# Kernel tuning notes

Measured on AMD Instinct MI355X. Metric: run time of the kernel, lower is better.

The kernel has to match this reference:

```python
import jax, jax.numpy as jnp
import numpy as np

N_NODES = 50000
N_EDGES = 500000


def setup_inputs() -> dict:
    key = jax.random.key(0)
    ks = jax.random.split(key, 24)
    p = {}
    p['x_feat'] = jax.random.normal(ks[0], (N_NODES, 24), dtype=jnp.float32)
    p['edge_index'] = jax.random.randint(ks[1], (2, N_EDGES), 0, N_NODES)
    p['edge_attr'] = jax.random.uniform(ks[2], (N_EDGES, 16), dtype=jnp.float32)
    def lin(k, fan_in, shape):
        b = 1.0 / np.sqrt(fan_in)
        return jax.random.uniform(k, shape, jnp.float32, -b, b)
    # group-0 input projection: 24 -> 32
    p['lin_prep_W'] = lin(ks[3], 24, (24, 32)); p['lin_prep_b'] = lin(ks[4], 24, (32,))
    # prep tube: 32 -> 16
    p['tube_W'] = lin(ks[5], 32, (32, 16)); p['tube_b'] = lin(ks[6], 32, (16,))
    # shared edge-attr trunk: 16 -> 32 -> 16
    p['edge_W1'] = lin(ks[7], 16, (16, 32)); p['edge_b1'] = lin(ks[8], 16, (32,))
    p['edge_W2'] = lin(ks[9], 32, (32, 16)); p['edge_b2'] = lin(ks[10], 32, (16,))
    # conv1: in=16, out=8 per aggr (mean, max, add)
    p['conv1_edge_W'] = lin(ks[11], 16, (3, 16, 16 * 8)); p['conv1_edge_b'] = lin(ks[12], 16, (3, 16 * 8))
    p['conv1_root_W'] = lin(ks[13], 16, (3, 16, 8)); p['conv1_bias'] = lin(ks[14], 16, (3, 8))
    # conv2: in=24, out=8 per aggr
    p['conv2_edge_W'] = lin(ks[15], 16, (3, 16, 24 * 8)); p['conv2_edge_b'] = lin(ks[16], 16, (3, 24 * 8))
    p['conv2_root_W'] = lin(ks[17], 24, (3, 24, 8)); p['conv2_bias'] = lin(ks[18], 24, (3, 8))
    # output head: 24 -> 2
    p['out_W'] = lin(ks[19], 24, (24, 2)); p['out_b'] = lin(ks[20], 24, (2,))
    return p


def _nnconv(x, e_repr, src, dst, edge_W, edge_b, root_W, bias, n_nodes):
    # x: [N, in]; e_repr: [E, 16]; edge_W: [3, 16, in*out]
    d_in = x.shape[1]
    x_src = x[src]  # [E, in]
    deg = jax.ops.segment_sum(jnp.ones_like(src, dtype=x.dtype), dst, num_segments=n_nodes)  # [N]
    outs = []
    for a, aggr in enumerate(('mean', 'max', 'add')):
        W_e = (e_repr @ edge_W[a] + edge_b[a]).reshape(e_repr.shape[0], d_in, -1)  # [E, in, out]
        msg = jnp.einsum('ei,eio->eo', x_src, W_e)  # [E, out]
        if aggr == 'add':
            agg = jax.ops.segment_sum(msg, dst, num_segments=n_nodes)
        elif aggr == 'mean':
            agg = jax.ops.segment_sum(msg, dst, num_segments=n_nodes) / jnp.maximum(deg, 1.0)[:, None]
        else:
            agg = jax.ops.segment_max(msg, dst, num_segments=n_nodes)
            agg = jnp.where(deg[:, None] > 0, agg, 0.0)  # no-neighbor nodes -> 0
        outs.append(agg + x @ root_W[a] + bias[a])
    return jax.nn.relu(jnp.concatenate(outs, axis=1))  # [N, 3*out]


def reference(x_feat, edge_index, edge_attr, lin_prep_W, lin_prep_b, tube_W, tube_b,
              edge_W1, edge_b1, edge_W2, edge_b2,
              conv1_edge_W, conv1_edge_b, conv1_root_W, conv1_bias,
              conv2_edge_W, conv2_edge_b, conv2_root_W, conv2_bias,
              out_W, out_b):
    n_nodes = x_feat.shape[0]
    src, dst = edge_index[0], edge_index[1]
    # node prep: group projection + tube (relu acts, dropout=0 -> identity)
    x = jax.nn.relu(x_feat @ lin_prep_W + lin_prep_b)       # [N, 32]
    x = jax.nn.relu(x @ tube_W + tube_b)                    # [N, 16]
    # shared edge-attr trunk (last activation = sigmoid), computed once
    e = jax.nn.relu(edge_attr @ edge_W1 + edge_b1)
    e_repr = jax.nn.sigmoid(e @ edge_W2 + edge_b2)          # [E, 16]
    # hop 1 and hop 2 of edge-conditioned NNConv with mean/max/add aggregators
    x = _nnconv(x, e_repr, src, dst, conv1_edge_W, conv1_edge_b, conv1_root_W, conv1_bias, n_nodes)  # [N, 24]
    x = _nnconv(x, e_repr, src, dst, conv2_edge_W, conv2_edge_b, conv2_root_W, conv2_bias, n_nodes)  # [N, 24]
    logits = x @ out_W + out_b                              # [N, 2]
    scores = jax.nn.softmax(logits, axis=1)
    return (logits, scores)
```

## Files before the change

### kernel.cpp

```cpp
#include <hip/hip_runtime.h>

#define BS 256

__device__ __forceinline__ unsigned short f2bf(float f) {
    unsigned x = __float_as_uint(f);
    return (unsigned short)((x + 0x7fffu + ((x >> 16) & 1u)) >> 16);
}
__device__ __forceinline__ unsigned pack2bf(float a, float b) {
    return (unsigned)f2bf(a) | ((unsigned)f2bf(b) << 16);
}
__device__ __forceinline__ void unpack2(unsigned u, float* d) {
    d[0] = __uint_as_float(u << 16);
    d[1] = __uint_as_float(u & 0xFFFF0000u);
}
__device__ __forceinline__ void unpack8(uint4 v, float* d) {
    unpack2(v.x, d); unpack2(v.y, d + 2); unpack2(v.z, d + 4); unpack2(v.w, d + 6);
}
__device__ __forceinline__ uint4 pack8bf(const float* r) {
    return make_uint4(pack2bf(r[0], r[1]), pack2bf(r[2], r[3]),
                      pack2bf(r[4], r[5]), pack2bf(r[6], r[7]));
}

__global__ void prep_kernel(const float* __restrict__ xf,
                            const float* __restrict__ W1, const float* __restrict__ b1,
                            const float* __restrict__ W2, const float* __restrict__ b2,
                            float* __restrict__ x16, int N)
{
    int n = blockIdx.x * blockDim.x + threadIdx.x;
    bool valid = n < N;
    int nn = valid ? n : 0;
    float a[24];
#pragma unroll
    for (int i = 0; i < 24; i += 4)
        *(float4*)(a + i) = *(const float4*)(xf + (size_t)nn * 24 + i);
    float h[32];
#pragma unroll
    for (int j = 0; j < 32; j++) {
        float s = b1[j];
#pragma unroll
        for (int i = 0; i < 24; i++) s = fmaf(a[i], W1[i * 32 + j], s);
        h[j] = fmaxf(s, 0.f);
    }
    if (!valid) return;
#pragma unroll
    for (int j = 0; j < 16; j++) {
        float s = b2[j];
#pragma unroll
        for (int i = 0; i < 32; i++) s = fmaf(h[i], W2[i * 16 + j], s);
        x16[(size_t)n * 16 + j] = fmaxf(s, 0.f);
    }
}

__global__ void degjj_kernel(const int* __restrict__ srcA, const int* __restrict__ dstA,
                             int* __restrict__ cntS, int* __restrict__ cntD,
                             int* __restrict__ jS, int* __restrict__ jD, int E)
{
    int base = blockIdx.x * (BS * 4) + threadIdx.x;
    int e0 = base, e1 = base + BS, e2 = base + 2 * BS, e3 = base + 3 * BS;
    bool v0 = e0 < E, v1 = e1 < E, v2 = e2 < E, v3 = e3 < E;
    int s0 = 0, s1 = 0, s2 = 0, s3 = 0, d0 = 0, d1 = 0, d2 = 0, d3 = 0;
    if (v0) { s0 = srcA[e0]; d0 = dstA[e0]; }
    if (v1) { s1 = srcA[e1]; d1 = dstA[e1]; }
    if (v2) { s2 = srcA[e2]; d2 = dstA[e2]; }
    if (v3) { s3 = srcA[e3]; d3 = dstA[e3]; }
    int a0 = 0, a1 = 0, a2 = 0, a3 = 0, b0 = 0, b1 = 0, b2 = 0, b3 = 0;
    if (v0) { a0 = atomicAdd(&cntS[s0], 1); b0 = atomicAdd(&cntD[d0], 1); }
    if (v1) { a1 = atomicAdd(&cntS[s1], 1); b1 = atomicAdd(&cntD[d1], 1); }
    if (v2) { a2 = atomicAdd(&cntS[s2], 1); b2 = atomicAdd(&cntD[d2], 1); }
    if (v3) { a3 = atomicAdd(&cntS[s3], 1); b3 = atomicAdd(&cntD[d3], 1); }
    if (v0) { jS[e0] = a0; jD[e0] = b0; }
    if (v1) { jS[e1] = a1; jD[e1] = b1; }
    if (v2) { jS[e2] = a2; jD[e2] = b2; }
    if (v3) { jS[e3] = a3; jD[e3] = b3; }
}

__global__ void offsets2_kernel(const int* __restrict__ cntS, const int* __restrict__ cntD,
                                int* __restrict__ offsS, int* __restrict__ offsD,
                                int* __restrict__ cursS, int* __restrict__ cursD, int N)
{
    int n = blockIdx.x * blockDim.x + threadIdx.x;
    int lane = threadIdx.x & 63;
    bool valid = n < N;
    int dS = valid ? cntS[n] : 0;
    int dD = valid ? cntD[n] : 0;
    int sS = dS, sD = dD;
#pragma unroll
    for (int o = 1; o < 64; o <<= 1) {
        int tS = __shfl_up(sS, o);
        int tD = __shfl_up(sD, o);
        if (lane >= o) { sS += tS; sD += tD; }
    }
    int totS = __shfl(sS, 63);
    int totD = __shfl(sD, 63);
    int baseS = 0, baseD = 0;
    if (lane == 63) {
        baseS = atomicAdd(cursS, totS);
        baseD = atomicAdd(cursD, totD);
    }
    baseS = __shfl(baseS, 63);
    baseD = __shfl(baseD, 63);
    if (valid) {
        offsS[n] = baseS + sS - dS;
        offsD[n] = baseD + sD - dD;
    }
}

__global__ __launch_bounds__(BS) void er_fill_kernel(
    const int* __restrict__ srcA, const int* __restrict__ dstA,
    const int* __restrict__ jS, const int* __restrict__ jD,
    const int* __restrict__ offsS, const int* __restrict__ offsD,
    const float* __restrict__ eattr,
    const float* __restrict__ eW1, const float* __restrict__ eb1,
    const float* __restrict__ eW2, const float* __restrict__ eb2,
    uint4* __restrict__ erec, int E)
{
    int e = blockIdx.x * BS + threadIdx.x;
    if (e >= E) return;
    int s = srcA[e], d = dstA[e];
    int p = offsS[s] + jS[e];
    int q = offsD[d] + jD[e];

    float ea[16];
#pragma unroll
    for (int i = 0; i < 16; i += 4)
        *(float4*)(ea + i) = *(const float4*)(eattr + (size_t)e * 16 + i);
    float h[32];
#pragma unroll
    for (int j = 0; j < 32; j++) {
        float t = eb1[j];
#pragma unroll
        for (int i = 0; i < 16; i++) t = fmaf(ea[i], eW1[i * 32 + j], t);
        h[j] = fmaxf(t, 0.f);
    }
    float er[16];
#pragma unroll
    for (int j = 0; j < 16; j++) {
        float t = eb2[j];
#pragma unroll
        for (int i = 0; i < 32; i++) t = fmaf(h[i], eW2[i * 16 + j], t);
        er[j] = 1.f / (1.f + __expf(-t));
    }
    unsigned w[8];
#pragma unroll
    for (int j = 0; j < 8; j++) w[j] = pack2bf(er[2 * j], er[2 * j + 1]);
    uint4* rp = erec + (size_t)p * 4;
    rp[0] = make_uint4((unsigned)s, (unsigned)q, w[0], w[1]);
    rp[1] = make_uint4(w[2], w[3], w[4], w[5]);
    rp[2] = make_uint4(w[6], w[7], 0u, 0u);
    rp[3] = make_uint4(0u, 0u, 0u, 0u);
}

template <int IN>
__global__ __launch_bounds__(BS) void ynode_kernel(const float* __restrict__ x,
                                                   const float* __restrict__ W,
                                                   const float* __restrict__ B,
                                                   const float* __restrict__ RW,
                                                   const float* __restrict__ RB,
                                                   unsigned short* __restrict__ Y,
                                                   float* __restrict__ root, int N)
{
    __shared__ float w_lds[IN * 24];
    int t = threadIdx.x;
    int k = blockIdx.y;

    for (int idx = t; idx < IN * 24; idx += BS) {
        int i = idx / 24;
        int j = idx - i * 24;
        int a = j >> 3, o = j & 7;
        float v;
        if (k < 16)       v = W[(((size_t)a * 16 + k) * IN + i) * 8 + o];
        else if (k == 16) v = B[((size_t)a * IN + i) * 8 + o];
        else              v = RW[((size_t)a * IN + i) * 8 + o];
        w_lds[idx] = v;
    }
    __syncthreads();

    int tid = blockIdx.x * BS + t;
    int n = tid / 3;
    int a = tid - n * 3;
    if (n >= N) return;

    float xv[IN];
#pragma unroll
    for (int i = 0; i < IN; i += 4)
        *(float4*)(xv + i) = *(const float4*)(x + (size_t)n * IN + i);

    float acc[8];
#pragma unroll
    for (int o = 0; o < 8; o++) acc[o] = 0.f;
    const float* wb = w_lds + a * 8;
#pragma unroll
    for (int i = 0; i < IN; i++) {
        float xi = xv[i];
#pragma unroll
        for (int o = 0; o < 8; o++)
            acc[o] = fmaf(xi, wb[i * 24 + o], acc[o]);
    }

    if (k < 17) {
        *(uint4*)(Y + ((size_t)k * N + n) * 24 + a * 8) = pack8bf(acc);
    } else {
        float* pr = root + (size_t)n * 24 + a * 8;
        *(float4*)(pr)     = make_float4(acc[0] + RB[a*8+0], acc[1] + RB[a*8+1],
                                         acc[2] + RB[a*8+2], acc[3] + RB[a*8+3]);
        *(float4*)(pr + 4) = make_float4(acc[4] + RB[a*8+4], acc[5] + RB[a*8+5],
                                         acc[6] + RB[a*8+6], acc[7] + RB[a*8+7]);
    }
}

__global__ __launch_bounds__(BS) void msg_kernel(
    const uint4* __restrict__ erec,
    const unsigned short* __restrict__ Y,
    unsigned short* __restrict__ msg16,
    int N, int E)
{
    int tid = blockIdx.x * BS + threadIdx.x;
    int p = tid / 3;
    int j = tid - p * 3;
    if (p >= E) return;

    const uint4* rp = erec + (size_t)p * 4;
    uint4 r0 = rp[0];
    uint4 r1 = rp[1];
    uint4 r2 = rp[2];
    unsigned s = r0.x, q = r0.y;

    float er[16];
    unpack2(r0.z, er); unpack2(r0.w, er + 2);
    unpack8(r1, er + 4);
    unpack2(r2.x, er + 12); unpack2(r2.y, er + 14);

    const unsigned short* yb = Y + (size_t)s * 24 + j * 8;
    size_t kstride = (size_t)N * 24;

    float acc[8];
    unpack8(*(const uint4*)(yb + 16 * kstride), acc);
#pragma unroll
    for (int k = 0; k < 16; k++) {
        float t[8];
        unpack8(*(const uint4*)(yb + (size_t)k * kstride), t);
        float ek = er[k];
#pragma unroll
        for (int o = 0; o < 8; o++) acc[o] = fmaf(ek, t[o], acc[o]);
    }
    unsigned short* mrow = msg16 + (size_t)q * 32;
    *(uint4*)(mrow + j * 8) = pack8bf(acc);
    if (j == 0) *(uint4*)(mrow + 24) = make_uint4(0, 0, 0, 0);
}

__global__ __launch_bounds__(BS) void gather_kernel(
    const unsigned short* __restrict__ msg16,
    const int* __restrict__ offs,
    const int* __restrict__ degi,
    const float* __restrict__ root,
    float* __restrict__ out, int N)
{
    int n = (blockIdx.x * BS + threadIdx.x) >> 6;
    if (n >= N) return;
    int lane = threadIdx.x & 63;
    int c = lane & 3;
    int r = lane >> 2;

    int off = offs[n];
    int d = degi[n];

    float s[8], m[8];
#pragma unroll
    for (int o = 0; o < 8; o++) { s[o] = 0.f; m[o] = -3.402823466e38f; }

    if (c < 3) {
        const unsigned short* base = msg16 + (size_t)off * 32 + c * 8;
        for (int j = r; j < d; j += 16) {
            uint4 v = *(const uint4*)(base + (size_t)j * 32);
            float t[8];
            unpack8(v, t);
#pragma unroll
            for (int o = 0; o < 8; o++) {
                s[o] += t[o];
                m[o] = fmaxf(m[o], t[o]);
            }
        }
    }
#pragma unroll
    for (int mask = 4; mask < 64; mask <<= 1) {
#pragma unroll
        for (int o = 0; o < 8; o++) {
            s[o] += __shfl_xor(s[o], mask);
            m[o] = fmaxf(m[o], __shfl_xor(m[o], mask));
        }
    }
    if (lane >= 3) return;

    float inv = 1.f / fmaxf((float)d, 1.f);
    const float* pr = root + (size_t)n * 24 + c * 8;
    float4 r0 = *(const float4*)(pr);
    float4 r1 = *(const float4*)(pr + 4);
    float rb[8] = {r0.x, r0.y, r0.z, r0.w, r1.x, r1.y, r1.z, r1.w};
    float rr[8];
#pragma unroll
    for (int o = 0; o < 8; o++) {
        float agg = (c == 0) ? s[o] * inv
                  : (c == 1) ? ((d > 0) ? m[o] : 0.f)
                  : s[o];
        rr[o] = fmaxf(rb[o] + agg, 0.f);
    }
    float* po = out + (size_t)n * 24 + c * 8;
    *(float4*)(po)     = make_float4(rr[0], rr[1], rr[2], rr[3]);
    *(float4*)(po + 4) = make_float4(rr[4], rr[5], rr[6], rr[7]);
}

__global__ void head_kernel(const float* __restrict__ x, const float* __restrict__ W,
                            const float* __restrict__ b, float* __restrict__ out, int N)
{
    int n = blockIdx.x * blockDim.x + threadIdx.x;
    if (n >= N) return;
    float l0 = b[0], l1 = b[1];
#pragma unroll
    for (int i = 0; i < 24; i++) {
        float xi = x[(size_t)n * 24 + i];
        l0 = fmaf(xi, W[i * 2 + 0], l0);
        l1 = fmaf(xi, W[i * 2 + 1], l1);
    }
    out[2 * (size_t)n + 0] = l0;
    out[2 * (size_t)n + 1] = l1;
    float mx = fmaxf(l0, l1);
    float e0 = __expf(l0 - mx), e1 = __expf(l1 - mx);
    float sm = e0 + e1;
    out[2 * (size_t)N + 2 * (size_t)n + 0] = e0 / sm;
    out[2 * (size_t)N + 2 * (size_t)n + 1] = e1 / sm;
}

extern "C" void kernel_launch(void* const* d_in, const int* in_sizes, int n_in,
                              void* d_out, int out_size, void* d_ws, size_t ws_size,
                              hipStream_t stream)
{
    const float* x_feat = (const float*)d_in[0];
    const int*   eidx   = (const int*)d_in[1];
    const float* eattr  = (const float*)d_in[2];
    const float* lpW = (const float*)d_in[3];
    const float* lpb = (const float*)d_in[4];
    const float* tW  = (const float*)d_in[5];
    const float* tb  = (const float*)d_in[6];
    const float* eW1 = (const float*)d_in[7];
    const float* eb1 = (const float*)d_in[8];
    const float* eW2 = (const float*)d_in[9];
    const float* eb2 = (const float*)d_in[10];
    const float* c1W = (const float*)d_in[11];
    const float* c1B = (const float*)d_in[12];
    const float* c1R = (const float*)d_in[13];
    const float* c1b = (const float*)d_in[14];
    const float* c2W = (const float*)d_in[15];
    const float* c2B = (const float*)d_in[16];
    const float* c2R = (const float*)d_in[17];
    const float* c2b = (const float*)d_in[18];
    const float* oW  = (const float*)d_in[19];
    const float* ob  = (const float*)d_in[20];

    int N = in_sizes[0] / 24;
    int E = in_sizes[1] / 2;
    const int* srcA = eidx;
    const int* dstA = eidx + E;

    char* wsb = (char*)d_ws;
    size_t off = 0;
    auto alloc = [&](size_t bytes) {
        off = (off + 255) & ~(size_t)255;
        void* p = wsb + off;
        off += bytes;
        return p;
    };
    unsigned short* Y     = (unsigned short*)alloc((size_t)17 * N * 24 * 2);
    unsigned short* msg16 = (unsigned short*)alloc((size_t)E * 32 * 2);
    uint4* erec = (uint4*)alloc((size_t)E * 64);
    float* root = (float*)alloc((size_t)N * 24 * 4);
    float* x16  = (float*)alloc((size_t)N * 16 * 4);
    float* x24a = (float*)alloc((size_t)N * 24 * 4);
    float* x24b = (float*)alloc((size_t)N * 24 * 4);
    int* ibase  = (int*)alloc(((size_t)2 * N + 2) * 4);
    int* cntS = ibase;
    int* cntD = ibase + N;
    int* cursS = ibase + 2 * N;
    int* cursD = ibase + 2 * N + 1;
    int* offsS = (int*)alloc((size_t)N * 4);
    int* offsD = (int*)alloc((size_t)N * 4);
    int* jS    = (int*)alloc((size_t)E * 4);
    int* jD    = (int*)alloc((size_t)E * 4);

    dim3 blk(BS);
    int nb_nodes = (N + BS - 1) / BS;
    int nb_edges = (E + BS - 1) / BS;
    int nb_deg   = (E + BS * 4 - 1) / (BS * 4);
    int nb_msg   = (3 * E + BS - 1) / BS;
    int nb_gath  = ((size_t)N * 64 + BS - 1) / BS;
    int nb_y3    = (3 * N + BS - 1) / BS;
    dim3 ygrid(nb_y3, 18);

    hipMemsetAsync(ibase, 0, (2 * (size_t)N + 2) * 4, stream);

    prep_kernel<<<nb_nodes, blk, 0, stream>>>(x_feat, lpW, lpb, tW, tb, x16, N);

    degjj_kernel<<<nb_deg, blk, 0, stream>>>(srcA, dstA, cntS, cntD, jS, jD, E);
    offsets2_kernel<<<nb_nodes, blk, 0, stream>>>(cntS, cntD, offsS, offsD, cursS, cursD, N);
    er_fill_kernel<<<nb_edges, blk, 0, stream>>>(srcA, dstA, jS, jD, offsS, offsD,
                                                 eattr, eW1, eb1, eW2, eb2, erec, E);

    ynode_kernel<16><<<ygrid, blk, 0, stream>>>(x16, c1W, c1B, c1R, c1b, Y, root, N);
    msg_kernel<<<nb_msg, blk, 0, stream>>>(erec, Y, msg16, N, E);
    gather_kernel<<<nb_gath, blk, 0, stream>>>(msg16, offsD, cntD, root, x24a, N);

    ynode_kernel<24><<<ygrid, blk, 0, stream>>>(x24a, c2W, c2B, c2R, c2b, Y, root, N);
    msg_kernel<<<nb_msg, blk, 0, stream>>>(erec, Y, msg16, N, E);
    gather_kernel<<<nb_gath, blk, 0, stream>>>(msg16, offsD, cntD, root, x24b, N);

    head_kernel<<<nb_nodes, blk, 0, stream>>>(x24b, oW, ob, (float*)d_out, N);
}
```

Measured before the change: 284.9 us.

## Fuse prep with degree counting, head into final gather, and batch edge MLP

Merges the node prep MLP and the degree/rank atomic counting into one launch, split by block index. The degree counting now uses one atomic per thread over 2E threads instead of four edges per thread. The output head and softmax are folded into the second gather kernel through cross-lane shuffles, which removes one launch and the x24b round trip. The edge MLP kernel now handles two edges per thread so each weight load is reused, at the cost of more registers per thread.

```diff
diff --git a/kernel.cpp b/kernel.cpp
--- a/kernel.cpp
+++ b/kernel.cpp
@@ -21,57 +21,49 @@
                       pack2bf(r[4], r[5]), pack2bf(r[6], r[7]));
 }
 
-__global__ void prep_kernel(const float* __restrict__ xf,
-                            const float* __restrict__ W1, const float* __restrict__ b1,
-                            const float* __restrict__ W2, const float* __restrict__ b2,
-                            float* __restrict__ x16, int N)
-{
-    int n = blockIdx.x * blockDim.x + threadIdx.x;
-    bool valid = n < N;
-    int nn = valid ? n : 0;
-    float a[24];
-#pragma unroll
-    for (int i = 0; i < 24; i += 4)
-        *(float4*)(a + i) = *(const float4*)(xf + (size_t)nn * 24 + i);
-    float h[32];
-#pragma unroll
-    for (int j = 0; j < 32; j++) {
-        float s = b1[j];
-#pragma unroll
-        for (int i = 0; i < 24; i++) s = fmaf(a[i], W1[i * 32 + j], s);
-        h[j] = fmaxf(s, 0.f);
-    }
-    if (!valid) return;
-#pragma unroll
-    for (int j = 0; j < 16; j++) {
-        float s = b2[j];
-#pragma unroll
-        for (int i = 0; i < 32; i++) s = fmaf(h[i], W2[i * 16 + j], s);
-        x16[(size_t)n * 16 + j] = fmaxf(s, 0.f);
-    }
-}
-
-__global__ void degjj_kernel(const int* __restrict__ srcA, const int* __restrict__ dstA,
-                             int* __restrict__ cntS, int* __restrict__ cntD,
-                             int* __restrict__ jS, int* __restrict__ jD, int E)
-{
-    int base = blockIdx.x * (BS * 4) + threadIdx.x;
-    int e0 = base, e1 = base + BS, e2 = base + 2 * BS, e3 = base + 3 * BS;
-    bool v0 = e0 < E, v1 = e1 < E, v2 = e2 < E, v3 = e3 < E;
-    int s0 = 0, s1 = 0, s2 = 0, s3 = 0, d0 = 0, d1 = 0, d2 = 0, d3 = 0;
-    if (v0) { s0 = srcA[e0]; d0 = dstA[e0]; }
-    if (v1) { s1 = srcA[e1]; d1 = dstA[e1]; }
-    if (v2) { s2 = srcA[e2]; d2 = dstA[e2]; }
-    if (v3) { s3 = srcA[e3]; d3 = dstA[e3]; }
-    int a0 = 0, a1 = 0, a2 = 0, a3 = 0, b0 = 0, b1 = 0, b2 = 0, b3 = 0;
-    if (v0) { a0 = atomicAdd(&cntS[s0], 1); b0 = atomicAdd(&cntD[d0], 1); }
-    if (v1) { a1 = atomicAdd(&cntS[s1], 1); b1 = atomicAdd(&cntD[d1], 1); }
-    if (v2) { a2 = atomicAdd(&cntS[s2], 1); b2 = atomicAdd(&cntD[d2], 1); }
-    if (v3) { a3 = atomicAdd(&cntS[s3], 1); b3 = atomicAdd(&cntD[d3], 1); }
-    if (v0) { jS[e0] = a0; jD[e0] = b0; }
-    if (v1) { jS[e1] = a1; jD[e1] = b1; }
-    if (v2) { jS[e2] = a2; jD[e2] = b2; }
-    if (v3) { jS[e3] = a3; jD[e3] = b3; }
+__global__ __launch_bounds__(BS) void prep_deg_kernel(
+    const float* __restrict__ xf,
+    const float* __restrict__ W1, const float* __restrict__ b1,
+    const float* __restrict__ W2, const float* __restrict__ b2,
+    float* __restrict__ x16,
+    const int* __restrict__ srcA, const int* __restrict__ dstA,
+    int* __restrict__ cntS, int* __restrict__ cntD,
+    int* __restrict__ jS, int* __restrict__ jD,
+    int N, int E, int nbPrep)
+{
+    if ((int)blockIdx.x < nbPrep) {
+        int n = blockIdx.x * BS + threadIdx.x;
+        bool valid = n < N;
+        int nn = valid ? n : 0;
+        float a[24];
+#pragma unroll
+        for (int i = 0; i < 24; i += 4)
+            *(float4*)(a + i) = *(const float4*)(xf + (size_t)nn * 24 + i);
+        float h[32];
+#pragma unroll
+        for (int j = 0; j < 32; j++) {
+            float s = b1[j];
+#pragma unroll
+            for (int i = 0; i < 24; i++) s = fmaf(a[i], W1[i * 32 + j], s);
+            h[j] = fmaxf(s, 0.f);
+        }
+        if (!valid) return;
+#pragma unroll
+        for (int j = 0; j < 16; j++) {
+            float s = b2[j];
+#pragma unroll
+            for (int i = 0; i < 32; i++) s = fmaf(h[i], W2[i * 16 + j], s);
+            x16[(size_t)n * 16 + j] = fmaxf(s, 0.f);
+        }
+    } else {
+        int tid = (blockIdx.x - nbPrep) * BS + threadIdx.x;
+        if (tid < E) {
+            jS[tid] = atomicAdd(&cntS[srcA[tid]], 1);
+        } else if (tid < 2 * E) {
+            int e = tid - E;
+            jD[e] = atomicAdd(&cntD[dstA[e]], 1);
+        }
+    }
 }
 
 __global__ void offsets2_kernel(const int* __restrict__ cntS, const int* __restrict__ cntD,
@@ -114,40 +106,72 @@
     const float* __restrict__ eW2, const float* __restrict__ eb2,
     uint4* __restrict__ erec, int E)
 {
-    int e = blockIdx.x * BS + threadIdx.x;
-    if (e >= E) return;
-    int s = srcA[e], d = dstA[e];
-    int p = offsS[s] + jS[e];
-    int q = offsD[d] + jD[e];
-
-    float ea[16];
-#pragma unroll
-    for (int i = 0; i < 16; i += 4)
-        *(float4*)(ea + i) = *(const float4*)(eattr + (size_t)e * 16 + i);
-    float h[32];
+    int e0 = blockIdx.x * (BS * 2) + threadIdx.x;
+    int e1 = e0 + BS;
+    bool v0 = e0 < E, v1 = e1 < E;
+    int f0 = v0 ? e0 : 0, f1 = v1 ? e1 : 0;
+
+    int s0 = srcA[f0], d0 = dstA[f0];
+    int s1 = srcA[f1], d1 = dstA[f1];
+    int p0 = offsS[s0] + jS[f0];
+    int q0 = offsD[d0] + jD[f0];
+    int p1 = offsS[s1] + jS[f1];
+    int q1 = offsD[d1] + jD[f1];
+
+    float ea0[16], ea1[16];
+#pragma unroll
+    for (int i = 0; i < 16; i += 4) {
+        *(float4*)(ea0 + i) = *(const float4*)(eattr + (size_t)f0 * 16 + i);
+        *(float4*)(ea1 + i) = *(const float4*)(eattr + (size_t)f1 * 16 + i);
+    }
+    float h0[32], h1[32];
 #pragma unroll
     for (int j = 0; j < 32; j++) {
-        float t = eb1[j];
-#pragma unroll
-        for (int i = 0; i < 16; i++) t = fmaf(ea[i], eW1[i * 32 + j], t);
-        h[j] = fmaxf(t, 0.f);
-    }
-    float er[16];
-#pragma unroll
-    for (int j = 0; j < 16; j++) {
-        float t = eb2[j];
-#pragma unroll
-        for (int i = 0; i < 32; i++) t = fmaf(h[i], eW2[i * 16 + j], t);
-        er[j] = 1.f / (1.f + __expf(-t));
-    }
-    unsigned w[8];
-#pragma unroll
-    for (int j = 0; j < 8; j++) w[j] = pack2bf(er[2 * j], er[2 * j + 1]);
-    uint4* rp = erec + (size_t)p * 4;
-    rp[0] = make_uint4((unsigned)s, (unsigned)q, w[0], w[1]);
-    rp[1] = make_uint4(w[2], w[3], w[4], w[5]);
-    rp[2] = make_uint4(w[6], w[7], 0u, 0u);
-    rp[3] = make_uint4(0u, 0u, 0u, 0u);
+        float t0 = eb1[j], t1 = t0;
+#pragma unroll
+        for (int i = 0; i < 16; i++) {
+            float w = eW1[i * 32 + j];
+            t0 = fmaf(ea0[i], w, t0);
+            t1 = fmaf(ea1[i], w, t1);
+        }
+        h0[j] = fmaxf(t0, 0.f);
+        h1[j] = fmaxf(t1, 0.f);
+    }
+    unsigned w0[8], w1[8];
+#pragma unroll
+    for (int j = 0; j < 16; j += 2) {
+        float ta = eb2[j], tb = ta;
+        float tc = eb2[j + 1], td = tc;
+#pragma unroll
+        for (int i = 0; i < 32; i++) {
+            float wa = eW2[i * 16 + j];
+            float wb = eW2[i * 16 + j + 1];
+            ta = fmaf(h0[i], wa, ta);
+            tb = fmaf(h1[i], wa, tb);
+            tc = fmaf(h0[i], wb, tc);
+            td = fmaf(h1[i], wb, td);
+        }
+        float era = 1.f / (1.f + __expf(-ta));
+        float erb = 1.f / (1.f + __expf(-tb));
+        float erc = 1.f / (1.f + __expf(-tc));
+        float erd = 1.f / (1.f + __expf(-td));
+        w0[j >> 1] = pack2bf(era, erc);
+        w1[j >> 1] = pack2bf(erb, erd);
+    }
+    if (v0) {
+        uint4* rp = erec + (size_t)p0 * 4;
+        rp[0] = make_uint4((unsigned)s0, (unsigned)q0, w0[0], w0[1]);
+        rp[1] = make_uint4(w0[2], w0[3], w0[4], w0[5]);
+        rp[2] = make_uint4(w0[6], w0[7], 0u, 0u);
+        rp[3] = make_uint4(0u, 0u, 0u, 0u);
+    }
+    if (v1) {
+        uint4* rp = erec + (size_t)p1 * 4;
+        rp[0] = make_uint4((unsigned)s1, (unsigned)q1, w1[0], w1[1]);
+        rp[1] = make_uint4(w1[2], w1[3], w1[4], w1[5]);
+        rp[2] = make_uint4(w1[6], w1[7], 0u, 0u);
+        rp[3] = make_uint4(0u, 0u, 0u, 0u);
+    }
 }
 
 template <int IN>
@@ -248,12 +272,15 @@
     if (j == 0) *(uint4*)(mrow + 24) = make_uint4(0, 0, 0, 0);
 }
 
+template <bool FUSE_HEAD>
 __global__ __launch_bounds__(BS) void gather_kernel(
     const unsigned short* __restrict__ msg16,
     const int* __restrict__ offs,
     const int* __restrict__ degi,
     const float* __restrict__ root,
-    float* __restrict__ out, int N)
+    float* __restrict__ out,
+    const float* __restrict__ oW, const float* __restrict__ ob,
+    int N)
 {
     int n = (blockIdx.x * BS + threadIdx.x) >> 6;
     if (n >= N) return;
@@ -289,45 +316,52 @@
             m[o] = fmaxf(m[o], __shfl_xor(m[o], mask));
         }
     }
-    if (lane >= 3) return;
-
-    float inv = 1.f / fmaxf((float)d, 1.f);
-    const float* pr = root + (size_t)n * 24 + c * 8;
-    float4 r0 = *(const float4*)(pr);
-    float4 r1 = *(const float4*)(pr + 4);
-    float rb[8] = {r0.x, r0.y, r0.z, r0.w, r1.x, r1.y, r1.z, r1.w};
+
+    bool active = (lane < 3);
     float rr[8];
-#pragma unroll
-    for (int o = 0; o < 8; o++) {
-        float agg = (c == 0) ? s[o] * inv
-                  : (c == 1) ? ((d > 0) ? m[o] : 0.f)
-                  : s[o];
-        rr[o] = fmaxf(rb[o] + agg, 0.f);
-    }
-    float* po = out + (size_t)n * 24 + c * 8;
-    *(float4*)(po)     = make_float4(rr[0], rr[1], rr[2], rr[3]);
-    *(float4*)(po + 4) = make_float4(rr[4], rr[5], rr[6], rr[7]);
-}
-
-__global__ void head_kernel(const float* __restrict__ x, const float* __restrict__ W,
-                            const float* __restrict__ b, float* __restrict__ out, int N)
-{
-    int n = blockIdx.x * blockDim.x + threadIdx.x;
-    if (n >= N) return;
-    float l0 = b[0], l1 = b[1];
-#pragma unroll
-    for (int i = 0; i < 24; i++) {
-        float xi = x[(size_t)n * 24 + i];
-        l0 = fmaf(xi, W[i * 2 + 0], l0);
-        l1 = fmaf(xi, W[i * 2 + 1], l1);
-    }
-    out[2 * (size_t)n + 0] = l0;
-    out[2 * (size_t)n + 1] = l1;
-    float mx = fmaxf(l0, l1);
-    float e0 = __expf(l0 - mx), e1 = __expf(l1 - mx);
-    float sm = e0 + e1;
-    out[2 * (size_t)N + 2 * (size_t)n + 0] = e0 / sm;
-    out[2 * (size_t)N + 2 * (size_t)n + 1] = e1 / sm;
+    if (active) {
+        float inv = 1.f / fmaxf((float)d, 1.f);
+        const float* pr = root + (size_t)n * 24 + lane * 8;
+        float4 r0 = *(const float4*)(pr);
+        float4 r1 = *(const float4*)(pr + 4);
+        float rb[8] = {r0.x, r0.y, r0.z, r0.w, r1.x, r1.y, r1.z, r1.w};
+#pragma unroll
+        for (int o = 0; o < 8; o++) {
+            float agg = (lane == 0) ? s[o] * inv
+                      : (lane == 1) ? ((d > 0) ? m[o] : 0.f)
+                      : s[o];
+            rr[o] = fmaxf(rb[o] + agg, 0.f);
+        }
+    }
+
+    if (!FUSE_HEAD) {
+        if (active) {
+            float* po = out + (size_t)n * 24 + lane * 8;
+            *(float4*)(po)     = make_float4(rr[0], rr[1], rr[2], rr[3]);
+            *(float4*)(po + 4) = make_float4(rr[4], rr[5], rr[6], rr[7]);
+        }
+    } else {
+        float l0p = 0.f, l1p = 0.f;
+        if (active) {
+#pragma unroll
+            for (int o = 0; o < 8; o++) {
+                l0p = fmaf(rr[o], oW[(lane * 8 + o) * 2 + 0], l0p);
+                l1p = fmaf(rr[o], oW[(lane * 8 + o) * 2 + 1], l1p);
+            }
+        }
+        float l0 = __shfl(l0p, 0) + __shfl(l0p, 1) + __shfl(l0p, 2);
+        float l1 = __shfl(l1p, 0) + __shfl(l1p, 1) + __shfl(l1p, 2);
+        if (lane == 0) {
+            l0 += ob[0]; l1 += ob[1];
+            out[2 * (size_t)n + 0] = l0;
+            out[2 * (size_t)n + 1] = l1;
+            float mx = fmaxf(l0, l1);
+            float e0 = __expf(l0 - mx), e1 = __expf(l1 - mx);
+            float sm = e0 + e1;
+            out[2 * (size_t)N + 2 * (size_t)n + 0] = e0 / sm;
+            out[2 * (size_t)N + 2 * (size_t)n + 1] = e1 / sm;
+        }
+    }
 }
 
 extern "C" void kernel_launch(void* const* d_in, const int* in_sizes, int n_in,
@@ -375,7 +409,6 @@
     float* root = (float*)alloc((size_t)N * 24 * 4);
     float* x16  = (float*)alloc((size_t)N * 16 * 4);
     float* x24a = (float*)alloc((size_t)N * 24 * 4);
-    float* x24b = (float*)alloc((size_t)N * 24 * 4);
     int* ibase  = (int*)alloc(((size_t)2 * N + 2) * 4);
     int* cntS = ibase;
     int* cntD = ibase + N;
@@ -388,8 +421,8 @@
 
     dim3 blk(BS);
     int nb_nodes = (N + BS - 1) / BS;
-    int nb_edges = (E + BS - 1) / BS;
-    int nb_deg   = (E + BS * 4 - 1) / (BS * 4);
+    int nb_deg2  = (2 * E + BS - 1) / BS;
+    int nb_fill  = (E + BS * 2 - 1) / (BS * 2);
     int nb_msg   = (3 * E + BS - 1) / BS;
     int nb_gath  = ((size_t)N * 64 + BS - 1) / BS;
     int nb_y3    = (3 * N + BS - 1) / BS;
@@ -397,20 +430,20 @@
 
     hipMemsetAsync(ibase, 0, (2 * (size_t)N + 2) * 4, stream);
 
-    prep_kernel<<<nb_nodes, blk, 0, stream>>>(x_feat, lpW, lpb, tW, tb, x16, N);
-
-    degjj_kernel<<<nb_deg, blk, 0, stream>>>(srcA, dstA, cntS, cntD, jS, jD, E);
+    prep_deg_kernel<<<nb_nodes + nb_deg2, blk, 0, stream>>>(
+        x_feat, lpW, lpb, tW, tb, x16, srcA, dstA, cntS, cntD, jS, jD, N, E, nb_nodes);
+
     offsets2_kernel<<<nb_nodes, blk, 0, stream>>>(cntS, cntD, offsS, offsD, cursS, cursD, N);
-    er_fill_kernel<<<nb_edges, blk, 0, stream>>>(srcA, dstA, jS, jD, offsS, offsD,
-                                                 eattr, eW1, eb1, eW2, eb2, erec, E);
+    er_fill_kernel<<<nb_fill, blk, 0, stream>>>(srcA, dstA, jS, jD, offsS, offsD,
+                                                eattr, eW1, eb1, eW2, eb2, erec, E);
 
     ynode_kernel<16><<<ygrid, blk, 0, stream>>>(x16, c1W, c1B, c1R, c1b, Y, root, N);
     msg_kernel<<<nb_msg, blk, 0, stream>>>(erec, Y, msg16, N, E);
-    gather_kernel<<<nb_gath, blk, 0, stream>>>(msg16, offsD, cntD, root, x24a, N);
+    gather_kernel<false><<<nb_gath, blk, 0, stream>>>(msg16, offsD, cntD, root, x24a,
+                                                      oW, ob, N);
 
     ynode_kernel<24><<<ygrid, blk, 0, stream>>>(x24a, c2W, c2B, c2R, c2b, Y, root, N);
     msg_kernel<<<nb_msg, blk, 0, stream>>>(erec, Y, msg16, N, E);
-    gather_kernel<<<nb_gath, blk, 0, stream>>>(msg16, offsD, cntD, root, x24b, N);
-
-    head_kernel<<<nb_nodes, blk, 0, stream>>>(x24b, oW, ob, (float*)d_out, N);
-}
+    gather_kernel<true><<<nb_gath, blk, 0, stream>>>(msg16, offsD, cntD, root,
+                                                     (float*)d_out, oW, ob, N);
+}
```

After: 530.7 us. 1.86x slower.
